# Kernel tuning notes

Hardware: AMD Instinct MI355X
Metric: run time of the kernel (lower is better)

Reference implementation:

```python
import jax, jax.numpy as jnp
import numpy as np

CODEBOOK_SIZE = 8192
CODEBOOK_DIM = 1024
HIDDEN_DIM = 4096
OUT_DIM = 1024
B, M = 32, 576


def setup_inputs() -> dict:
    key = jax.random.key(0)
    k_idx, k_cb, k_w1, k_w2 = jax.random.split(key, 4)
    index = jax.random.randint(k_idx, (B, M), 0, CODEBOOK_SIZE, dtype=jnp.int32)
    # codebook initialized as sqrt(d) * randn, as in the torch module
    codebook = (CODEBOOK_DIM ** 0.5) * jax.random.normal(k_cb, (CODEBOOK_SIZE, CODEBOOK_DIM), dtype=jnp.float32)
    s1 = 1.0 / np.sqrt(CODEBOOK_DIM)
    s2 = 1.0 / np.sqrt(HIDDEN_DIM)
    W1 = s1 * jax.random.normal(k_w1, (CODEBOOK_DIM, HIDDEN_DIM), dtype=jnp.float32)
    b1 = jnp.zeros((HIDDEN_DIM,), dtype=jnp.float32)
    W2 = s2 * jax.random.normal(k_w2, (HIDDEN_DIM, OUT_DIM), dtype=jnp.float32)
    b2 = jnp.zeros((OUT_DIM,), dtype=jnp.float32)
    return {"index": index, "codebook": codebook, "W1": W1, "b1": b1, "W2": W2, "b2": b2}


def reference(index, codebook, W1, b1, W2, b2):
    # one_hot(index) @ codebook is mathematically an index gather:
    # quantized[b, m, :] = codebook[index[b, m], :]
    quantized = jnp.take(codebook, index, axis=0)  # [B, M, D]
    # Decoder_ff: 2-layer GELU MLP (D -> 4D -> D)
    h = jax.nn.gelu(jnp.einsum('bmd,dh->bmh', quantized, W1) + b1)
    rec = jnp.einsum('bmh,ho->bmo', h, W2) + b2
    return rec
```

## Files before the change

### kernel.cpp

```cpp
#include <hip/hip_runtime.h>
#include <stdint.h>

typedef __attribute__((ext_vector_type(8))) short s16x8;
typedef __attribute__((ext_vector_type(4))) float f32x4;

__device__ __forceinline__ short f2bf(float x) {
  uint32_t u = __builtin_bit_cast(uint32_t, x);
  u += 0x7FFFu + ((u >> 16) & 1u);
  return (short)(u >> 16);
}

__device__ __forceinline__ void gload16(void* l, const void* g) {
  __builtin_amdgcn_global_load_lds(
      (const __attribute__((address_space(1))) void*)g,
      (__attribute__((address_space(3))) void*)l, 16, 0, 0);
}

__device__ __forceinline__ float gelu_tanh(float x) {
  float u = 0.7978845608028654f * (x + 0.044715f * x * x * x);
  float e = __expf(2.0f * u);
  return x - x / (e + 1.0f);
}

__global__ void gather_cvt(const float* __restrict__ cb, const int* __restrict__ idx,
                           short* __restrict__ out) {
  int m = blockIdx.x * 2 + (threadIdx.x >> 7);
  int c = (threadIdx.x & 127) * 8;
  const float* s = cb + (size_t)idx[m] * 1024 + c;
  s16x8 o;
#pragma unroll
  for (int j = 0; j < 8; ++j) o[j] = f2bf(s[j]);
  *(s16x8*)(out + (size_t)m * 1024 + c) = o;
}

__global__ void cvt_T(const float* __restrict__ in, short* __restrict__ out, int K, int N) {
  int Kb = K >> 3;
  int t = blockIdx.x * 256 + threadIdx.x;
  if (t >= N * Kb) return;
  int n = t / Kb;
  int k8 = (t - n * Kb) * 8;
  const float* s = in + (size_t)k8 * N + n;
  s16x8 o;
#pragma unroll
  for (int j = 0; j < 8; ++j) o[j] = f2bf(s[(size_t)j * N]);
  *(s16x8*)(out + (size_t)n * K + k8) = o;
}

template <int MODE, int K, int N>
__global__ __launch_bounds__(512, 2) void gemm2p(
    const short* __restrict__ A, const short* __restrict__ Bt,
    const float* __restrict__ bias, void* __restrict__ Cv) {
  constexpr int BM = 144, BN = 256;
  constexpr int ATS = BM * 64;
  constexpr int LDSH = (BM + BN) * 64;
  __shared__ short lds[2 * LDSH + 512];

  constexpr int NBN = N / BN;
  const int nwg = gridDim.x;
  int swz = blockIdx.x;
  swz = (swz & 7) * (nwg >> 3) + (swz >> 3);
  const int bm = swz / NBN, bn = swz - (swz / NBN) * NBN;

  const int tid = threadIdx.x;
  const int wid = tid >> 6, lane = tid & 63;
  const int lr = lane & 15, hi = lane >> 4;

  const int sl = (tid & 7) ^ ((tid >> 3) & 7);
  const long rstep = (long)64 * K;
  const short* aptr0 = A + (long)(bm * BM + (tid >> 3)) * K + sl * 8;
  const short* aptrP = A + (long)(bm * BM + 128 + ((tid >> 3) & 15)) * K + sl * 8;
  const short* bptr0 = Bt + (long)(bn * BN + (tid >> 3)) * K + sl * 8;
  const int wlds = wid * 512;

  const int aRB = lr * 64;
  const int bRB = ATS + (wid * 32 + lr) * 64;
  const int sk0 = (hi ^ (lr & 7)) * 8;
  const int sk1 = ((4 + hi) ^ (lr & 7)) * 8;

  f32x4 acc[9][2] = {};
  s16x8 af[5][2], bf[2][2];

  constexpr int NT = K >> 6;

#pragma unroll
  for (int r = 0; r < 4; ++r) gload16(&lds[ATS + r * 4096 + wlds], bptr0 + r * rstep);
  gload16(&lds[0 + wlds], aptr0);
  gload16(&lds[4096 + wlds], aptr0 + rstep);
  gload16((wid < 2) ? &lds[8192 + wlds] : &lds[2 * LDSH], aptrP);
  asm volatile("s_waitcnt vmcnt(2)" ::: "memory");
  __builtin_amdgcn_s_barrier();

  for (int t = 0; t < NT; ++t) {
    const int cb = (t & 1) * LDSH;
    const int nb = LDSH - cb;
    const int kt = ((t + 1 < NT) ? (t + 1) : 0) << 6;

#pragma unroll
    for (int mi = 0; mi < 4; ++mi) {
      af[mi][0] = *(const s16x8*)&lds[cb + aRB + mi * 1024 + sk0];
      af[mi][1] = *(const s16x8*)&lds[cb + aRB + mi * 1024 + sk1];
    }
#pragma unroll
    for (int nj = 0; nj < 2; ++nj) {
      bf[nj][0] = *(const s16x8*)&lds[cb + bRB + nj * 1024 + sk0];
      bf[nj][1] = *(const s16x8*)&lds[cb + bRB + nj * 1024 + sk1];
    }
#pragma unroll
    for (int r = 0; r < 4; ++r)
      gload16(&lds[nb + ATS + r * 4096 + wlds], bptr0 + r * rstep + kt);
    __builtin_amdgcn_s_barrier();
    asm volatile("s_waitcnt lgkmcnt(0)" ::: "memory");
    __builtin_amdgcn_s_setprio(1);
#pragma unroll
    for (int mi = 0; mi < 4; ++mi)
#pragma unroll
      for (int nj = 0; nj < 2; ++nj)
#pragma unroll
        for (int ks = 0; ks < 2; ++ks)
          acc[mi][nj] = __builtin_amdgcn_mfma_f32_16x16x32_bf16(af[mi][ks], bf[nj][ks], acc[mi][nj], 0, 0, 0);
    __builtin_amdgcn_s_setprio(0);
    asm volatile("s_waitcnt vmcnt(4)" ::: "memory");
    __builtin_amdgcn_s_barrier();

#pragma unroll
    for (int mi = 0; mi < 5; ++mi) {
      af[mi][0] = *(const s16x8*)&lds[cb + aRB + (4 + mi) * 1024 + sk0];
      af[mi][1] = *(const s16x8*)&lds[cb + aRB + (4 + mi) * 1024 + sk1];
    }
    gload16(&lds[nb + 0 + wlds], aptr0 + kt);
    gload16(&lds[nb + 4096 + wlds], aptr0 + rstep + kt);
    gload16((wid < 2) ? &lds[nb + 8192 + wlds] : &lds[2 * LDSH], aptrP + kt);
    __builtin_amdgcn_s_barrier();
    asm volatile("s_waitcnt lgkmcnt(0)" ::: "memory");
    __builtin_amdgcn_s_setprio(1);
#pragma unroll
    for (int mi = 0; mi < 5; ++mi)
#pragma unroll
      for (int nj = 0; nj < 2; ++nj)
#pragma unroll
        for (int ks = 0; ks < 2; ++ks)
          acc[4 + mi][nj] = __builtin_amdgcn_mfma_f32_16x16x32_bf16(af[mi][ks], bf[nj][ks], acc[4 + mi][nj], 0, 0, 0);
    __builtin_amdgcn_s_setprio(0);
    asm volatile("s_waitcnt vmcnt(2)" ::: "memory");
    __builtin_amdgcn_s_barrier();
  }

  const int m0 = bm * BM + hi * 4;
  const int n0 = bn * BN + wid * 32 + lr;
#pragma unroll
  for (int nj = 0; nj < 2; ++nj) {
    const int n = n0 + nj * 16;
    const float bv = bias[n];
#pragma unroll
    for (int mi = 0; mi < 9; ++mi) {
      f32x4 v = acc[mi][nj];
#pragma unroll
      for (int r = 0; r < 4; ++r) {
        const int m = m0 + mi * 16 + r;
        float x = v[r] + bv;
        if (MODE == 1) {
          ((short*)Cv)[(size_t)m * N + n] = f2bf(gelu_tanh(x));
        } else {
          ((float*)Cv)[(size_t)m * N + n] = x;
        }
      }
    }
  }
}

extern "C" void kernel_launch(void* const* d_in, const int* in_sizes, int n_in,
                              void* d_out, int out_size, void* d_ws, size_t ws_size,
                              hipStream_t stream) {
  const int* idx = (const int*)d_in[0];
  const float* cb = (const float*)d_in[1];
  const float* W1 = (const float*)d_in[2];
  const float* b1 = (const float*)d_in[3];
  const float* W2 = (const float*)d_in[4];
  const float* b2 = (const float*)d_in[5];
  float* out = (float*)d_out;

  const int Mtot = 32 * 576;

  char* ws = (char*)d_ws;
  short* aq = (short*)(ws);
  short* w1t = (short*)(ws + (size_t)40 * 1024 * 1024);
  short* w2t = (short*)(ws + (size_t)48 * 1024 * 1024);
  short* h = (short*)(ws + (size_t)56 * 1024 * 1024);

  gather_cvt<<<Mtot / 2, 256, 0, stream>>>(cb, idx, aq);
  cvt_T<<<2048, 256, 0, stream>>>(W1, w1t, 1024, 4096);
  cvt_T<<<2048, 256, 0, stream>>>(W2, w2t, 4096, 1024);

  size_t avail = (ws_size > (size_t)56 * 1024 * 1024) ? ws_size - (size_t)56 * 1024 * 1024 : 0;
  int nc = 1;
  while (nc < 8 && (size_t)(Mtot / nc) * 8192 > avail) nc <<= 1;
  const int Mc = Mtot / nc;

  for (int c = 0; c < nc; ++c) {
    gemm2p<1, 1024, 4096><<<(Mc / 144) * 16, 512, 0, stream>>>(
        aq + (size_t)c * Mc * 1024, w1t, b1, (void*)h);
    gemm2p<2, 4096, 1024><<<(Mc / 144) * 4, 512, 0, stream>>>(
        h, w2t, b2, (void*)(out + (size_t)c * Mc * 1024));
  }
}
```

Before: 475.0 us.

## Triple-buffer LDS in the GEMM with prefetch distance two and one barrier per tile

Moves the bf16 GEMM from double to triple LDS buffering. Global-to-LDS loads for tile t+2 are issued while tile t is computed, and the read, spare and write buffers rotate each iteration. This cuts the per-tile barriers from four to one and waits only on the loads for the next tile, so global latency is better hidden and wave stalls drop. In exchange, LDS use grows to about 154KB per workgroup, which rules out a second resident workgroup on a CU. The tail iterations also issue redundant loads.

```diff
diff --git a/kernel.cpp b/kernel.cpp
--- a/kernel.cpp
+++ b/kernel.cpp
@@ -47,13 +47,13 @@
 }
 
 template <int MODE, int K, int N>
-__global__ __launch_bounds__(512, 2) void gemm2p(
+__global__ __launch_bounds__(512, 2) void gemm3b(
     const short* __restrict__ A, const short* __restrict__ Bt,
     const float* __restrict__ bias, void* __restrict__ Cv) {
   constexpr int BM = 144, BN = 256;
   constexpr int ATS = BM * 64;
   constexpr int LDSH = (BM + BN) * 64;
-  __shared__ short lds[2 * LDSH + 512];
+  __shared__ short lds[3 * LDSH + 512];
 
   constexpr int NBN = N / BN;
   const int nwg = gridDim.x;
@@ -71,6 +71,8 @@
   const short* aptrP = A + (long)(bm * BM + 128 + ((tid >> 3) & 15)) * K + sl * 8;
   const short* bptr0 = Bt + (long)(bn * BN + (tid >> 3)) * K + sl * 8;
   const int wlds = wid * 512;
+  const bool realP = (wid < 2);
+  constexpr int SCR = 3 * LDSH;
 
   const int aRB = lr * 64;
   const int bRB = ATS + (wid * 32 + lr) * 64;
@@ -83,32 +85,35 @@
   constexpr int NT = K >> 6;
 
 #pragma unroll
-  for (int r = 0; r < 4; ++r) gload16(&lds[ATS + r * 4096 + wlds], bptr0 + r * rstep);
-  gload16(&lds[0 + wlds], aptr0);
-  gload16(&lds[4096 + wlds], aptr0 + rstep);
-  gload16((wid < 2) ? &lds[8192 + wlds] : &lds[2 * LDSH], aptrP);
-  asm volatile("s_waitcnt vmcnt(2)" ::: "memory");
+  for (int tt = 0; tt < 2; ++tt) {
+    const int wb = tt * LDSH, kk = tt * 64;
+#pragma unroll
+    for (int r = 0; r < 4; ++r) gload16(&lds[wb + ATS + r * 4096 + wlds], bptr0 + r * rstep + kk);
+    gload16(&lds[wb + 0 + wlds], aptr0 + kk);
+    gload16(&lds[wb + 4096 + wlds], aptr0 + rstep + kk);
+    gload16(realP ? &lds[wb + 8192 + wlds] : &lds[SCR], aptrP + kk);
+  }
+  asm volatile("s_waitcnt vmcnt(7)" ::: "memory");
   __builtin_amdgcn_s_barrier();
 
+  int rb0 = 0, rb1 = LDSH, rb2 = 2 * LDSH;
+
   for (int t = 0; t < NT; ++t) {
-    const int cb = (t & 1) * LDSH;
-    const int nb = LDSH - cb;
-    const int kt = ((t + 1 < NT) ? (t + 1) : 0) << 6;
+    const int kt = ((t + 2 < NT) ? (t + 2) : t) << 6;
 
 #pragma unroll
     for (int mi = 0; mi < 4; ++mi) {
-      af[mi][0] = *(const s16x8*)&lds[cb + aRB + mi * 1024 + sk0];
-      af[mi][1] = *(const s16x8*)&lds[cb + aRB + mi * 1024 + sk1];
+      af[mi][0] = *(const s16x8*)&lds[rb0 + aRB + mi * 1024 + sk0];
+      af[mi][1] = *(const s16x8*)&lds[rb0 + aRB + mi * 1024 + sk1];
     }
 #pragma unroll
     for (int nj = 0; nj < 2; ++nj) {
-      bf[nj][0] = *(const s16x8*)&lds[cb + bRB + nj * 1024 + sk0];
-      bf[nj][1] = *(const s16x8*)&lds[cb + bRB + nj * 1024 + sk1];
+      bf[nj][0] = *(const s16x8*)&lds[rb0 + bRB + nj * 1024 + sk0];
+      bf[nj][1] = *(const s16x8*)&lds[rb0 + bRB + nj * 1024 + sk1];
     }
 #pragma unroll
     for (int r = 0; r < 4; ++r)
-      gload16(&lds[nb + ATS + r * 4096 + wlds], bptr0 + r * rstep + kt);
-    __builtin_amdgcn_s_barrier();
+      gload16(&lds[rb2 + ATS + r * 4096 + wlds], bptr0 + r * rstep + kt);
     asm volatile("s_waitcnt lgkmcnt(0)" ::: "memory");
     __builtin_amdgcn_s_setprio(1);
 #pragma unroll
@@ -119,18 +124,15 @@
         for (int ks = 0; ks < 2; ++ks)
           acc[mi][nj] = __builtin_amdgcn_mfma_f32_16x16x32_bf16(af[mi][ks], bf[nj][ks], acc[mi][nj], 0, 0, 0);
     __builtin_amdgcn_s_setprio(0);
-    asm volatile("s_waitcnt vmcnt(4)" ::: "memory");
-    __builtin_amdgcn_s_barrier();
 
 #pragma unroll
     for (int mi = 0; mi < 5; ++mi) {
-      af[mi][0] = *(const s16x8*)&lds[cb + aRB + (4 + mi) * 1024 + sk0];
-      af[mi][1] = *(const s16x8*)&lds[cb + aRB + (4 + mi) * 1024 + sk1];
-    }
-    gload16(&lds[nb + 0 + wlds], aptr0 + kt);
-    gload16(&lds[nb + 4096 + wlds], aptr0 + rstep + kt);
-    gload16((wid < 2) ? &lds[nb + 8192 + wlds] : &lds[2 * LDSH], aptrP + kt);
-    __builtin_amdgcn_s_barrier();
+      af[mi][0] = *(const s16x8*)&lds[rb0 + aRB + (4 + mi) * 1024 + sk0];
+      af[mi][1] = *(const s16x8*)&lds[rb0 + aRB + (4 + mi) * 1024 + sk1];
+    }
+    gload16(&lds[rb2 + 0 + wlds], aptr0 + kt);
+    gload16(&lds[rb2 + 4096 + wlds], aptr0 + rstep + kt);
+    gload16(realP ? &lds[rb2 + 8192 + wlds] : &lds[SCR], aptrP + kt);
     asm volatile("s_waitcnt lgkmcnt(0)" ::: "memory");
     __builtin_amdgcn_s_setprio(1);
 #pragma unroll
@@ -141,8 +143,10 @@
         for (int ks = 0; ks < 2; ++ks)
           acc[4 + mi][nj] = __builtin_amdgcn_mfma_f32_16x16x32_bf16(af[mi][ks], bf[nj][ks], acc[4 + mi][nj], 0, 0, 0);
     __builtin_amdgcn_s_setprio(0);
-    asm volatile("s_waitcnt vmcnt(2)" ::: "memory");
+
+    asm volatile("s_waitcnt vmcnt(7)" ::: "memory");
     __builtin_amdgcn_s_barrier();
+    const int tmp = rb0; rb0 = rb1; rb1 = rb2; rb2 = tmp;
   }
 
   const int m0 = bm * BM + hi * 4;
@@ -197,9 +201,9 @@
   const int Mc = Mtot / nc;
 
   for (int c = 0; c < nc; ++c) {
-    gemm2p<1, 1024, 4096><<<(Mc / 144) * 16, 512, 0, stream>>>(
+    gemm3b<1, 1024, 4096><<<(Mc / 144) * 16, 512, 0, stream>>>(
         aq + (size_t)c * Mc * 1024, w1t, b1, (void*)h);
-    gemm2p<2, 4096, 1024><<<(Mc / 144) * 4, 512, 0, stream>>>(
+    gemm3b<2, 4096, 1024><<<(Mc / 144) * 4, 512, 0, stream>>>(
         h, w2t, b2, (void*)(out + (size_t)c * Mc * 1024));
   }
 }
```

Result: faster. 419.6 us (-11.7%).
